# Performance work log

Measured on AMD Instinct MI355X. Metric: run time of the kernel, lower is better.

## Reference

```python
import jax, jax.numpy as jnp
import numpy as np

N, E = 50000, 800000          # nodes, edges
IN_DIM, HID, OUT = 200, 256, 64  # hidden_dims
R = 2                          # num_relations
NEG_SLOPE = 0.2                # RGATConv default negative_slope
EPS = 1e-16                    # PyG softmax denominator eps


def _glorot(key, shape, fan):
    return jax.random.normal(key, shape, dtype=jnp.float32) / np.float32(np.sqrt(fan))


def setup_inputs() -> dict:
    key = jax.random.key(0)
    ks = jax.random.split(key, 13)
    features = jax.random.normal(ks[0], (N, IN_DIM), dtype=jnp.float32)
    edge_index = jax.random.randint(ks[1], (2, E), 0, N, dtype=jnp.int64)
    edge_type = jax.random.randint(ks[2], (E,), 0, R, dtype=jnp.int64)
    return {
        "features": features,
        "edge_index": edge_index,
        "edge_type": edge_type,
        # RGATConv layer 1 (heads=1, dim=1): weight [R, in, out], q/k [out, 1]
        "w1": _glorot(ks[3], (R, IN_DIM, HID), IN_DIM),
        "q1": _glorot(ks[4], (HID, 1), HID),
        "k1": _glorot(ks[5], (HID, 1), HID),
        # RGATConv layer 2
        "w2": _glorot(ks[6], (R, HID, OUT), HID),
        "q2": _glorot(ks[7], (OUT, 1), OUT),
        "k2": _glorot(ks[8], (OUT, 1), OUT),
        # decoder: Linear(OUT->HID) then Linear(HID->IN_DIM), stored as [in, out]
        "dW1": _glorot(ks[9], (OUT, HID), OUT),
        "db1": jnp.zeros((HID,), jnp.float32),
        "dW2": _glorot(ks[10], (HID, IN_DIM), HID),
        "db2": jnp.zeros((IN_DIM,), jnp.float32),
    }


def rgat_conv(x, src, dst, etype, w, q, k):
    """PyG RGATConv: additive-self-attention, across-relation softmax,
    heads=1, dim=1, concat=False, bias=False, aggr=add (eval mode: no dropout)."""
    n = x.shape[0]
    # relation-specific transform at node level (per-edge bmm factors through nodes)
    xw = jnp.einsum('ni,ric->rnc', x, w)          # [R, N, C]
    qn = jnp.einsum('rnc,ch->rnh', xw, q)         # [R, N, 1]
    kn = jnp.einsum('rnc,ch->rnh', xw, k)         # [R, N, 1]
    # per-edge attention logit: leaky_relu(q_i + k_j)
    alpha = jax.nn.leaky_relu(qn[etype, dst] + kn[etype, src], NEG_SLOPE)  # [E, 1]
    # segment softmax over destination nodes (across relations)
    m = jax.lax.stop_gradient(jax.ops.segment_max(alpha, dst, num_segments=n))
    m = jnp.where(jnp.isfinite(m), m, jnp.float32(0.0))
    ea = jnp.exp(alpha - m[dst])
    denom = jax.ops.segment_sum(ea, dst, num_segments=n)
    att = ea / (denom[dst] + EPS)                 # [E, 1]
    # scatter-add weighted messages
    msg = att * xw[etype, src]                    # [E, C]
    return jax.ops.segment_sum(msg, dst, num_segments=n)  # [N, C]


def reference(features, edge_index, edge_type, w1, q1, k1, w2, q2, k2, dW1, db1, dW2, db2):
    src, dst = edge_index[0], edge_index[1]
    h1 = jax.nn.elu(rgat_conv(features, src, dst, edge_type, w1, q1, k1))
    h2 = jax.nn.elu(rgat_conv(h1, src, dst, edge_type, w2, q2, k2))
    h3 = (h2 @ dW1 + db1) @ dW2 + db2   # decoder (PCA mode: no ReLU)
    return (h2, h3)
```

## Files before the change

### kernel.cpp

```cpp
#include <hip/hip_runtime.h>

#define IN_DIM 200
#define HID    256
#define OUT_D  64
#define RREL   2
#define NEG_SLOPE 0.2f
#define NNODE  50000
#define MPAD   50048

typedef __attribute__((ext_vector_type(8))) short bf16x8;
typedef __attribute__((ext_vector_type(4))) float f32x4;
typedef __attribute__((ext_vector_type(4))) unsigned int u32x4;

__device__ __forceinline__ float bf2f(unsigned short u) {
    union { unsigned int i; float f; } v; v.i = ((unsigned int)u) << 16; return v.f;
}
__device__ __forceinline__ unsigned short f2bf(float f) {
    union { float f; unsigned int i; } v; v.f = f;
    unsigned int u = v.i;
    return (unsigned short)((u + 0x7FFFu + ((u >> 16) & 1u)) >> 16);
}
__device__ __forceinline__ float elu(float v) { return v > 0.f ? v : (__expf(v) - 1.0f); }

__global__ void feat_cvt(const float* __restrict__ in, unsigned short* __restrict__ out)
{
    long long idx = (long long)blockIdx.x * 256 + threadIdx.x;
    int row = (int)(idx >> 6);
    int c4  = ((int)idx & 63) << 2;
    if (row >= MPAD) return;
    unsigned short v[4];
    #pragma unroll
    for (int i = 0; i < 4; ++i) {
        int c = c4 + i;
        float f = (row < NNODE && c < IN_DIM) ? in[(long long)row * IN_DIM + c] : 0.f;
        v[i] = f2bf(f);
    }
    *(ushort4*)(out + (long long)row * 256 + c4) = make_ushort4(v[0], v[1], v[2], v[3]);
}

__global__ void wt_cvt(const float* __restrict__ in, unsigned short* __restrict__ out,
                       int Kreal, int Nreal, int Kpad, int Npad, int nb)
{
    long long total = (long long)nb * Npad * Kpad;
    long long idx = (long long)blockIdx.x * 256 + threadIdx.x;
    if (idx >= total) return;
    int kk = (int)(idx % Kpad);
    long long t = idx / Kpad;
    int nrow = (int)(t % Npad);
    int z = (int)(t / Npad);
    float f = (kk < Kreal && nrow < Nreal) ? in[((long long)z * Kreal + kk) * Nreal + nrow] : 0.f;
    out[idx] = f2bf(f);
}

__global__ void wt_cvt_stack(const float* __restrict__ in, unsigned short* __restrict__ out)
{
    int idx = blockIdx.x * 256 + threadIdx.x;
    if (idx >= 2 * 256 * 256) return;
    int kk = idx & 255;
    int c  = (idx >> 8) & 255;
    int z  = idx >> 16;
    float f = (kk < IN_DIM) ? in[((long long)z * IN_DIM + kk) * 256 + c] : 0.f;
    out[(long long)c * 512 + z * 256 + kk] = f2bf(f);
}

__global__ __launch_bounds__(256) void wqk_cvt(
    const float* __restrict__ w, const float* __restrict__ q,
    const float* __restrict__ k, float* __restrict__ wqv, float* __restrict__ wkv)
{
    int wv = ((blockIdx.x << 8) + threadIdx.x) >> 6;
    int lane = threadIdx.x & 63;
    if (wv >= 512) return;
    int r = wv >> 8, kk = wv & 255;
    float sq = 0.f, sk = 0.f;
    if (kk < IN_DIM) {
        const float* row = w + ((long long)(r * IN_DIM + kk)) * 256;
        float4 wv4 = *(const float4*)(row + lane * 4);
        float4 qv4 = *(const float4*)(q + lane * 4);
        float4 kv4 = *(const float4*)(k + lane * 4);
        sq = wv4.x * qv4.x + wv4.y * qv4.y + wv4.z * qv4.z + wv4.w * qv4.w;
        sk = wv4.x * kv4.x + wv4.y * kv4.y + wv4.z * kv4.z + wv4.w * kv4.w;
        #pragma unroll
        for (int off = 32; off; off >>= 1) {
            sq += __shfl_xor(sq, off);
            sk += __shfl_xor(sk, off);
        }
    }
    if (lane == 0) { wqv[r * 256 + kk] = sq; wkv[r * 256 + kk] = sk; }
}

__global__ __launch_bounds__(256) void qk_feat(
    const unsigned short* __restrict__ A1, const float* __restrict__ wqv,
    const float* __restrict__ wkv, float* __restrict__ qn, float* __restrict__ kn, int n)
{
    int wv = ((blockIdx.x << 8) + threadIdx.x) >> 6;
    int lane = threadIdx.x & 63;
    if (wv >= n) return;
    ushort4 v = *(const ushort4*)(A1 + (long long)wv * 256 + lane * 4);
    float x0 = bf2f(v.x), x1 = bf2f(v.y), x2 = bf2f(v.z), x3 = bf2f(v.w);
    float4 q0v = *(const float4*)(wqv + lane * 4);
    float4 k0v = *(const float4*)(wkv + lane * 4);
    float4 q1v = *(const float4*)(wqv + 256 + lane * 4);
    float4 k1v = *(const float4*)(wkv + 256 + lane * 4);
    float sq0 = x0 * q0v.x + x1 * q0v.y + x2 * q0v.z + x3 * q0v.w;
    float sk0 = x0 * k0v.x + x1 * k0v.y + x2 * k0v.z + x3 * k0v.w;
    float sq1 = x0 * q1v.x + x1 * q1v.y + x2 * q1v.z + x3 * q1v.w;
    float sk1 = x0 * k1v.x + x1 * k1v.y + x2 * k1v.z + x3 * k1v.w;
    #pragma unroll
    for (int off = 32; off; off >>= 1) {
        sq0 += __shfl_xor(sq0, off);
        sk0 += __shfl_xor(sk0, off);
        sq1 += __shfl_xor(sq1, off);
        sk1 += __shfl_xor(sk1, off);
    }
    if (lane == 0) {
        qn[wv] = sq0; qn[n + wv] = sq1;
        kn[wv] = sk0; kn[n + wv] = sk1;
    }
}

template<bool OUT_BF16, bool DO_ELU, bool FUSE_QK>
__global__ __launch_bounds__(256) void gemm_mfma(
    const unsigned short* __restrict__ A,
    const unsigned short* __restrict__ Bt,
    const float* __restrict__ bias,
    void* __restrict__ Cout,
    const float* __restrict__ qvec, const float* __restrict__ kvec,
    float* __restrict__ qn_out, float* __restrict__ kn_out,
    int M, int Nn, int Kp, int Npad,
    long long strideC)
{
    __shared__ __align__(16) char lds[49152];
    const int tid  = threadIdx.x;
    const int lane = tid & 63;
    const int w    = tid >> 6;
    const int m0   = blockIdx.x * 128;
    const int n0   = blockIdx.y * 64;
    const int z    = blockIdx.z;

    const char* Ab = (const char*)A;
    const char* Bb = (const char*)(Bt + (long long)z * Npad * Kp);
    const int rs = Kp * 2;

    f32x4 acc[2][4];
    #pragma unroll
    for (int i = 0; i < 2; ++i)
        #pragma unroll
        for (int j = 0; j < 4; ++j) acc[i][j] = (f32x4){0.f, 0.f, 0.f, 0.f};

    const int KT = Kp >> 6;

    auto stage = [&](int buf, int kt) {
        char* lA = lds + buf * 24576;
        char* lB = lA + 16384;
        #pragma unroll
        for (int i = 0; i < 4; ++i) {
            int g = i * 256 + tid;
            int row = g >> 3, c = g & 7;
            const char* src = Ab + (long long)(m0 + row) * rs + kt * 128 + ((c ^ (row & 7)) << 4);
            __builtin_amdgcn_global_load_lds((const __attribute__((address_space(1))) void*)src,
                                             (__attribute__((address_space(3))) void*)(lA + g * 16),
                                             16, 0, 0);
        }
        #pragma unroll
        for (int i = 0; i < 2; ++i) {
            int g = i * 256 + tid;
            int row = g >> 3, c = g & 7;
            const char* src = Bb + (long long)(n0 + row) * rs + kt * 128 + ((c ^ (row & 7)) << 4);
            __builtin_amdgcn_global_load_lds((const __attribute__((address_space(1))) void*)src,
                                             (__attribute__((address_space(3))) void*)(lB + g * 16),
                                             16, 0, 0);
        }
    };

    stage(0, 0);
    int cur = 0;
    for (int kt = 0; kt < KT; ++kt) {
        __syncthreads();
        if (kt + 1 < KT) stage(cur ^ 1, kt + 1);
        const char* lA = lds + cur * 24576;
        const char* lB = lA + 16384;
        #pragma unroll
        for (int ks = 0; ks < 2; ++ks) {
            const int kg = ks * 4 + (lane >> 4);
            bf16x8 a[2], b[4];
            #pragma unroll
            for (int mi = 0; mi < 2; ++mi) {
                int row = w * 32 + mi * 16 + (lane & 15);
                a[mi] = *(const bf16x8*)(lA + row * 128 + ((kg ^ (row & 7)) << 4));
            }
            #pragma unroll
            for (int nj = 0; nj < 4; ++nj) {
                int row = nj * 16 + (lane & 15);
                b[nj] = *(const bf16x8*)(lB + row * 128 + ((kg ^ (row & 7)) << 4));
            }
            #pragma unroll
            for (int mi = 0; mi < 2; ++mi)
                #pragma unroll
                for (int nj = 0; nj < 4; ++nj)
                    acc[mi][nj] = __builtin_amdgcn_mfma_f32_16x16x32_bf16(a[mi], b[nj], acc[mi][nj], 0, 0, 0);
        }
        cur ^= 1;
    }

    const int colb = n0 + (lane & 15);
    #pragma unroll
    for (int mi = 0; mi < 2; ++mi) {
        #pragma unroll
        for (int nj = 0; nj < 4; ++nj) {
            int col = colb + nj * 16;
            if (col >= Nn) continue;
            float badd = bias ? bias[col] : 0.f;
            #pragma unroll
            for (int r = 0; r < 4; ++r) {
                int rowm = m0 + w * 32 + mi * 16 + ((lane >> 4) << 2) + r;
                if (rowm >= M) continue;
                float v = acc[mi][nj][r] + badd;
                if (DO_ELU) v = v > 0.f ? v : (__expf(v) - 1.0f);
                if (OUT_BF16)
                    ((unsigned short*)Cout)[strideC * z + (long long)rowm * Nn + col] = f2bf(v);
                else
                    ((float*)Cout)[strideC * z + (long long)rowm * Nn + col] = v;
            }
        }
    }

    if (FUSE_QK) {
        float qv[4], kv[4];
        #pragma unroll
        for (int nj = 0; nj < 4; ++nj) {
            int col = colb + nj * 16;
            bool ok = col < Nn;
            qv[nj] = ok ? qvec[col] : 0.f;
            kv[nj] = ok ? kvec[col] : 0.f;
        }
        #pragma unroll
        for (int mi = 0; mi < 2; ++mi) {
            #pragma unroll
            for (int r = 0; r < 4; ++r) {
                float sq = 0.f, sk = 0.f;
                #pragma unroll
                for (int nj = 0; nj < 4; ++nj) {
                    sq = fmaf(acc[mi][nj][r], qv[nj], sq);
                    sk = fmaf(acc[mi][nj][r], kv[nj], sk);
                }
                #pragma unroll
                for (int off = 1; off < 16; off <<= 1) {
                    sq += __shfl_xor(sq, off);
                    sk += __shfl_xor(sk, off);
                }
                if ((lane & 15) == 0) {
                    int rowm = m0 + w * 32 + mi * 16 + ((lane >> 4) << 2) + r;
                    if (rowm < M) {
                        atomicAdd(qn_out + (long long)z * M + rowm, sq);
                        atomicAdd(kn_out + (long long)z * M + rowm, sk);
                    }
                }
            }
        }
    }
}

__global__ void count_kernel(const int* __restrict__ dst, const int* __restrict__ etype,
                             int* __restrict__ deg2, int E)
{
    int e = blockIdx.x * 256 + threadIdx.x;
    if (e < E) atomicAdd(&deg2[(dst[e] << 1) | etype[e]], 1);
}

__global__ __launch_bounds__(256) void scan_blocksum(
    const int* __restrict__ deg, int* __restrict__ bsum, int n)
{
    __shared__ int red[256];
    int i = blockIdx.x * 256 + threadIdx.x;
    int v = (i < n) ? deg[i] : 0;
    red[threadIdx.x] = v;
    __syncthreads();
    #pragma unroll
    for (int off = 128; off; off >>= 1) {
        if (threadIdx.x < off) red[threadIdx.x] += red[threadIdx.x + off];
        __syncthreads();
    }
    if (threadIdx.x == 0) bsum[blockIdx.x] = red[0];
}

__global__ __launch_bounds__(512) void scan_bsum(int* __restrict__ bsum, int nb)
{
    __shared__ int buf[512];
    const int t = threadIdx.x;
    int v = (t < nb) ? bsum[t] : 0;
    buf[t] = v;
    __syncthreads();
    #pragma unroll
    for (int off = 1; off < 512; off <<= 1) {
        int u = (t >= off) ? buf[t - off] : 0;
        __syncthreads();
        buf[t] += u;
        __syncthreads();
    }
    if (t < nb) bsum[t] = buf[t] - v;
}

__global__ __launch_bounds__(256) void scan_final(
    const int* __restrict__ deg, const int* __restrict__ bsum,
    int* __restrict__ row_ptr, int* __restrict__ cursor, int n)
{
    __shared__ int buf[256];
    const int t = threadIdx.x;
    const int i = blockIdx.x * 256 + t;
    int v = (i < n) ? deg[i] : 0;
    buf[t] = v;
    __syncthreads();
    #pragma unroll
    for (int off = 1; off < 256; off <<= 1) {
        int u = (t >= off) ? buf[t - off] : 0;
        __syncthreads();
        buf[t] += u;
        __syncthreads();
    }
    int excl = bsum[blockIdx.x] + buf[t] - v;
    if (i < n) { row_ptr[i] = excl; cursor[i] = excl; }
    if (i == n - 1) row_ptr[n] = excl + v;
}

__global__ void scatter_kernel(const int* __restrict__ dst, const int* __restrict__ src,
                               const int* __restrict__ etype, int* __restrict__ cursor2,
                               int* __restrict__ epk, int E)
{
    int e = blockIdx.x * 256 + threadIdx.x;
    if (e < E) {
        int p = atomicAdd(&cursor2[(dst[e] << 1) | etype[e]], 1);
        epk[p] = src[e];
    }
}

__global__ __launch_bounds__(256) void aggregate_z(
    const unsigned short* __restrict__ A1,
    const float* __restrict__ qn,
    const float* __restrict__ kn,
    const int* __restrict__ row_ptr2,
    const int* __restrict__ epk,
    unsigned short* __restrict__ z,
    int n)
{
    const int wv   = ((blockIdx.x << 8) + threadIdx.x) >> 6;
    const int lane = threadIdx.x & 63;
    if (wv >= n) return;
    const int d = wv;
    const int start = row_ptr2[2 * d];
    const int mid   = row_ptr2[2 * d + 1];
    const int end   = row_ptr2[2 * d + 2];
    const int cnt = end - start;
    const int c0  = mid - start;
    const float q0 = qn[d];
    const float q1 = qn[n + d];
    const int slot = lane >> 5;
    const int hl   = lane & 31;

    auto fma8 = [](float acc[8], float w, const u32x4& r) {
        #pragma unroll
        for (int t2 = 0; t2 < 4; ++t2) {
            unsigned dw = r[t2];
            acc[2 * t2]     = fmaf(w, __uint_as_float(dw << 16),         acc[2 * t2]);
            acc[2 * t2 + 1] = fmaf(w, __uint_as_float(dw & 0xFFFF0000u), acc[2 * t2 + 1]);
        }
    };

    if (cnt <= 64) {
        int pv = 0; float a = -INFINITY;
        if (lane < cnt) {
            pv = epk[start + lane];
            bool r1 = lane >= c0;
            a = (r1 ? q1 : q0) + kn[(r1 ? n : 0) + pv];
            a = a > 0.f ? a : NEG_SLOPE * a;
        }
        float mx = a;
        #pragma unroll
        for (int off = 32; off; off >>= 1) mx = fmaxf(mx, __shfl_xor(mx, off));
        float ev = (lane < cnt) ? __expf(a - mx) : 0.f;
        float se = ev;
        #pragma unroll
        for (int off = 32; off; off >>= 1) se += __shfl_xor(se, off);
        const float wvv = ev * (1.f / (se + 1e-16f));

        #pragma unroll
        for (int seg = 0; seg < 2; ++seg) {
            const int segoff = seg ? c0 : 0;
            const int cs = seg ? (cnt - c0) : c0;
            float accA[8], accB[8];
            #pragma unroll
            for (int i = 0; i < 8; ++i) { accA[i] = 0.f; accB[i] = 0.f; }

            const int iters = (cs + 1) >> 1;
            int k = 0;
            for (; k + 4 <= iters; k += 4) {
                const int e0 = slot + k * 2, e1 = e0 + 2, e2 = e0 + 4, e3 = e0 + 6;
                int   p0 = __shfl(pv, segoff + e0);
                float w0 = __shfl(wvv, segoff + e0);
                int   p1 = __shfl(pv, segoff + e1);
                float w1 = __shfl(wvv, segoff + e1);
                int   p2 = __shfl(pv, segoff + e2);
                float w2 = __shfl(wvv, segoff + e2);
                int   p3 = __shfl(pv, segoff + e3);
                float w3 = __shfl(wvv, segoff + e3);
                if (e0 >= cs) w0 = 0.f;
                if (e1 >= cs) w1 = 0.f;
                if (e2 >= cs) w2 = 0.f;
                if (e3 >= cs) w3 = 0.f;
                const u32x4 r0 = *(const u32x4*)(A1 + (long long)p0 * 256 + hl * 8);
                const u32x4 r1 = *(const u32x4*)(A1 + (long long)p1 * 256 + hl * 8);
                const u32x4 r2 = *(const u32x4*)(A1 + (long long)p2 * 256 + hl * 8);
                const u32x4 r3 = *(const u32x4*)(A1 + (long long)p3 * 256 + hl * 8);
                fma8(accA, w0, r0);
                fma8(accB, w1, r1);
                fma8(accA, w2, r2);
                fma8(accB, w3, r3);
            }
            for (; k < iters; ++k) {
                const int e0 = slot + k * 2;
                int   p0 = __shfl(pv, segoff + e0);
                float w0 = __shfl(wvv, segoff + e0);
                if (e0 >= cs) w0 = 0.f;
                const u32x4 r0 = *(const u32x4*)(A1 + (long long)p0 * 256 + hl * 8);
                fma8(accA, w0, r0);
            }

            float acc[8];
            #pragma unroll
            for (int i = 0; i < 8; ++i) acc[i] = accA[i] + accB[i];
            #pragma unroll
            for (int t2 = 0; t2 < 8; ++t2) acc[t2] += __shfl_xor(acc[t2], 32);
            if (slot == 0) {
                u32x4 pack;
                #pragma unroll
                for (int t2 = 0; t2 < 4; ++t2)
                    pack[t2] = (unsigned)f2bf(acc[2 * t2]) | ((unsigned)f2bf(acc[2 * t2 + 1]) << 16);
                *(u32x4*)(z + (long long)d * 512 + seg * 256 + hl * 8) = pack;
            }
        }
        return;
    }

    float mx = -INFINITY;
    for (int j = start + lane; j < end; j += 64) {
        int s = epk[j];
        bool r1 = j >= mid;
        float a = (r1 ? q1 : q0) + kn[(r1 ? n : 0) + s];
        a = a > 0.f ? a : NEG_SLOPE * a;
        mx = fmaxf(mx, a);
    }
    #pragma unroll
    for (int off = 32; off; off >>= 1) mx = fmaxf(mx, __shfl_xor(mx, off));

    float se = 0.f;
    for (int j = start + lane; j < end; j += 64) {
        int s = epk[j];
        bool r1 = j >= mid;
        float a = (r1 ? q1 : q0) + kn[(r1 ? n : 0) + s];
        a = a > 0.f ? a : NEG_SLOPE * a;
        se += __expf(a - mx);
    }
    #pragma unroll
    for (int off = 32; off; off >>= 1) se += __shfl_xor(se, off);
    const float inv = 1.f / (se + 1e-16f);

    #pragma unroll
    for (int seg = 0; seg < 2; ++seg) {
        const int s0 = seg ? mid : start;
        const int s1 = seg ? end : mid;
        const float qr = seg ? q1 : q0;
        const int kbase = seg ? n : 0;

        float accA[8], accB[8];
        #pragma unroll
        for (int i = 0; i < 8; ++i) { accA[i] = 0.f; accB[i] = 0.f; }

        for (int base = s0; base < s1; base += 64) {
            const int cnt2 = min(64, s1 - base);
            int pv = 0; float wvv = 0.f;
            if (lane < cnt2) {
                pv = epk[base + lane];
                float a = qr + kn[kbase + pv];
                a = a > 0.f ? a : NEG_SLOPE * a;
                wvv = __expf(a - mx) * inv;
            }
            const int iters = (cnt2 + 1) >> 1;
            int k = 0;
            for (; k + 2 <= iters; k += 2) {
                const int e0 = slot + k * 2;
                const int e1 = e0 + 2;
                int   pA = __shfl(pv, e0);
                float wA = __shfl(wvv, e0);
                int   pB = __shfl(pv, e1);
                float wB = __shfl(wvv, e1);
                const u32x4 rA = *(const u32x4*)(A1 + (long long)pA * 256 + hl * 8);
                const u32x4 rB = *(const u32x4*)(A1 + (long long)pB * 256 + hl * 8);
                fma8(accA, wA, rA);
                fma8(accB, wB, rB);
            }
            if (k < iters) {
                const int e0 = slot + k * 2;
                int   pA = __shfl(pv, e0);
                float wA = __shfl(wvv, e0);
                const u32x4 rA = *(const u32x4*)(A1 + (long long)pA * 256 + hl * 8);
                fma8(accA, wA, rA);
            }
        }

        float acc[8];
        #pragma unroll
        for (int i = 0; i < 8; ++i) acc[i] = accA[i] + accB[i];
        #pragma unroll
        for (int t2 = 0; t2 < 8; ++t2) acc[t2] += __shfl_xor(acc[t2], 32);

        if (slot == 0) {
            u32x4 pack;
            #pragma unroll
            for (int t2 = 0; t2 < 4; ++t2)
                pack[t2] = (unsigned)f2bf(acc[2 * t2]) | ((unsigned)f2bf(acc[2 * t2 + 1]) << 16);
            *(u32x4*)(z + (long long)d * 512 + seg * 256 + hl * 8) = pack;
        }
    }
}

__global__ __launch_bounds__(256) void aggregate2(
    const unsigned short* __restrict__ xw,
    const float* __restrict__ qn,
    const float* __restrict__ kn,
    const int* __restrict__ row_ptr2,
    const int* __restrict__ epk,
    unsigned short* __restrict__ outb,
    float* __restrict__ outf,
    int n)
{
    constexpr int LPE   = 8;
    constexpr int NSLOT = 8;

    const int wv   = ((blockIdx.x << 8) + threadIdx.x) >> 6;
    const int lane = threadIdx.x & 63;
    if (wv >= n) return;
    const int d = wv;
    const int start = row_ptr2[2 * d];
    const int mid   = row_ptr2[2 * d + 1];
    const int end   = row_ptr2[2 * d + 2];
    const int cnt = end - start;
    const int c0  = mid - start;
    const float q0 = qn[d];
    const float q1 = qn[n + d];
    const int slot = lane / LPE;
    const int hl   = lane % LPE;

    auto fma8 = [](float acc[8], float w, const u32x4& r) {
        #pragma unroll
        for (int t2 = 0; t2 < 4; ++t2) {
            unsigned dw = r[t2];
            acc[2 * t2]     = fmaf(w, __uint_as_float(dw << 16),         acc[2 * t2]);
            acc[2 * t2 + 1] = fmaf(w, __uint_as_float(dw & 0xFFFF0000u), acc[2 * t2 + 1]);
        }
    };

    float accA[8], accB[8];
    #pragma unroll
    for (int i = 0; i < 8; ++i) { accA[i] = 0.f; accB[i] = 0.f; }

    if (cnt <= 64) {
        int pv = 0; float a = -INFINITY;
        if (lane < cnt) {
            pv = epk[start + lane];
            bool r1 = lane >= c0;
            a = (r1 ? q1 : q0) + kn[(r1 ? n : 0) + pv];
            a = a > 0.f ? a : NEG_SLOPE * a;
        }
        float mx = a;
        #pragma unroll
        for (int off = 32; off; off >>= 1) mx = fmaxf(mx, __shfl_xor(mx, off));
        float ev = (lane < cnt) ? __expf(a - mx) : 0.f;
        float se = ev;
        #pragma unroll
        for (int off = 32; off; off >>= 1) se += __shfl_xor(se, off);
        const float wvn = ev * (1.f / (se + 1e-16f));

        const int iters = (cnt + NSLOT - 1) / NSLOT;
        int k = 0;
        for (; k + 2 <= iters; k += 2) {
            const int e0 = slot + k * NSLOT;
            const int e1 = e0 + NSLOT;
            int   pA = __shfl(pv, e0);
            float wA = __shfl(wvn, e0);
            int   pB = __shfl(pv, e1);
            float wB = __shfl(wvn, e1);
            const long long oA = ((e0 >= c0) ? (long long)MPAD * 64 : 0) + (long long)pA * 64 + hl * 8;
            const long long oB = ((e1 >= c0) ? (long long)MPAD * 64 : 0) + (long long)pB * 64 + hl * 8;
            const u32x4 rA = *(const u32x4*)(xw + oA);
            const u32x4 rB = *(const u32x4*)(xw + oB);
            fma8(accA, wA, rA);
            fma8(accB, wB, rB);
        }
        if (k < iters) {
            const int e0 = slot + k * NSLOT;
            int   pA = __shfl(pv, e0);
            float wA = __shfl(wvn, e0);
            const long long oA = ((e0 >= c0) ? (long long)MPAD * 64 : 0) + (long long)pA * 64 + hl * 8;
            const u32x4 rA = *(const u32x4*)(xw + oA);
            fma8(accA, wA, rA);
        }
    } else {
        float mx = -INFINITY;
        for (int j = start + lane; j < end; j += 64) {
            int s = epk[j];
            bool r1 = j >= mid;
            float a = (r1 ? q1 : q0) + kn[(r1 ? n : 0) + s];
            a = a > 0.f ? a : NEG_SLOPE * a;
            mx = fmaxf(mx, a);
        }
        #pragma unroll
        for (int off = 32; off; off >>= 1) mx = fmaxf(mx, __shfl_xor(mx, off));

        float se = 0.f;
        for (int j = start + lane; j < end; j += 64) {
            int s = epk[j];
            bool r1 = j >= mid;
            float a = (r1 ? q1 : q0) + kn[(r1 ? n : 0) + s];
            a = a > 0.f ? a : NEG_SLOPE * a;
            se += __expf(a - mx);
        }
        #pragma unroll
        for (int off = 32; off; off >>= 1) se += __shfl_xor(se, off);
        const float inv = 1.f / (se + 1e-16f);

        for (int base = start; base < end; base += 64) {
            const int cnt2 = min(64, end - base);
            int pv = 0; float wvn = 0.f;
            if (lane < cnt2) {
                int j = base + lane;
                pv = epk[j];
                bool r1 = j >= mid;
                float a = (r1 ? q1 : q0) + kn[(r1 ? n : 0) + pv];
                a = a > 0.f ? a : NEG_SLOPE * a;
                wvn = __expf(a - mx) * inv;
            }
            const int iters = (cnt2 + NSLOT - 1) / NSLOT;
            int k = 0;
            for (; k + 2 <= iters; k += 2) {
                const int e0 = slot + k * NSLOT;
                const int e1 = e0 + NSLOT;
                int   pA = __shfl(pv, e0);
                float wA = __shfl(wvn, e0);
                int   pB = __shfl(pv, e1);
                float wB = __shfl(wvn, e1);
                const long long oA = ((base + e0 >= mid) ? (long long)MPAD * 64 : 0) + (long long)pA * 64 + hl * 8;
                const long long oB = ((base + e1 >= mid) ? (long long)MPAD * 64 : 0) + (long long)pB * 64 + hl * 8;
                const u32x4 rA = *(const u32x4*)(xw + oA);
                const u32x4 rB = *(const u32x4*)(xw + oB);
                fma8(accA, wA, rA);
                fma8(accB, wB, rB);
            }
            if (k < iters) {
                const int e0 = slot + k * NSLOT;
                int   pA = __shfl(pv, e0);
                float wA = __shfl(wvn, e0);
                const long long oA = ((base + e0 >= mid) ? (long long)MPAD * 64 : 0) + (long long)pA * 64 + hl * 8;
                const u32x4 rA = *(const u32x4*)(xw + oA);
                fma8(accA, wA, rA);
            }
        }
    }

    float acc[8];
    #pragma unroll
    for (int i = 0; i < 8; ++i) acc[i] = accA[i] + accB[i];
    #pragma unroll
    for (int off = LPE; off < 64; off <<= 1)
        #pragma unroll
        for (int t2 = 0; t2 < 8; ++t2) acc[t2] += __shfl_xor(acc[t2], off);

    if (slot == 0) {
        float fo[8];
        #pragma unroll
        for (int t2 = 0; t2 < 8; ++t2) fo[t2] = elu(acc[t2]);
        u32x4 pack;
        #pragma unroll
        for (int t2 = 0; t2 < 4; ++t2)
            pack[t2] = (unsigned)f2bf(fo[2 * t2]) | ((unsigned)f2bf(fo[2 * t2 + 1]) << 16);
        *(u32x4*)(outb + (long long)d * 64 + hl * 8) = pack;
        *(float4*)(outf + (long long)d * 64 + hl * 8)     = make_float4(fo[0], fo[1], fo[2], fo[3]);
        *(float4*)(outf + (long long)d * 64 + hl * 8 + 4) = make_float4(fo[4], fo[5], fo[6], fo[7]);
    }
}

extern "C" void kernel_launch(void* const* d_in, const int* in_sizes, int n_in,
                              void* d_out, int out_size, void* d_ws, size_t ws_size,
                              hipStream_t stream)
{
    const float* features = (const float*)d_in[0];
    const int*   ei       = (const int*)d_in[1];
    const int*   etype    = (const int*)d_in[2];
    const float* w1       = (const float*)d_in[3];
    const float* q1       = (const float*)d_in[4];
    const float* k1       = (const float*)d_in[5];
    const float* w2       = (const float*)d_in[6];
    const float* q2       = (const float*)d_in[7];
    const float* k2       = (const float*)d_in[8];
    const float* dW1      = (const float*)d_in[9];
    const float* db1      = (const float*)d_in[10];
    const float* dW2      = (const float*)d_in[11];
    const float* db2      = (const float*)d_in[12];

    const int n = in_sizes[0] / IN_DIM;
    const int E = in_sizes[2];
    const int n2 = 2 * n;
    const int* src = ei;
    const int* dst = ei + E;

    float* out_h2 = (float*)d_out;
    float* out_h3 = out_h2 + (long long)n * OUT_D;

    char* wp = (char*)d_ws;
    auto carve = [&](size_t bytes) {
        char* p = wp; wp += (bytes + 255) & ~(size_t)255; return p;
    };
    unsigned short* A1   = (unsigned short*)carve((size_t)MPAD * 256 * 2);
    unsigned short* zbuf = (unsigned short*)carve((size_t)MPAD * 512 * 2);
    unsigned short* h1   = (unsigned short*)carve((size_t)MPAD * 256 * 2);
    unsigned short* xw2  = (unsigned short*)carve((size_t)2 * MPAD * 64 * 2);
    unsigned short* h2b  = (unsigned short*)carve((size_t)MPAD * 64 * 2);
    unsigned short* tdec = (unsigned short*)carve((size_t)MPAD * 256 * 2);
    unsigned short* wst  = (unsigned short*)carve((size_t)256 * 512 * 2);
    unsigned short* w2t  = (unsigned short*)carve((size_t)2 * 64 * 256 * 2);
    unsigned short* dW1t = (unsigned short*)carve((size_t)256 * 64 * 2);
    unsigned short* dW2t = (unsigned short*)carve((size_t)256 * 256 * 2);
    float* wqv    = (float*)carve((size_t)2 * 256 * 4);
    float* wkv    = (float*)carve((size_t)2 * 256 * 4);
    float* qnb    = (float*)carve((size_t)n2 * 4);
    float* knb    = (float*)carve((size_t)n2 * 4);
    int* row_ptr2 = (int*)carve((size_t)(n2 + 1) * 4);
    int* cursor2  = (int*)carve((size_t)n2 * 4);
    int* deg2     = (int*)carve((size_t)n2 * 4);
    int* bsum     = (int*)carve((size_t)512 * 4);
    int* epk      = (int*)carve((size_t)E * 4);

    const int EB  = (E + 255) / 256;
    const int NB2 = (n2 + 255) / 256;
    const int MB  = (n + 127) / 128;
    const int WAVE_N  = (n + 3) / 4;

    hipMemsetAsync(deg2, 0, (size_t)n2 * sizeof(int), stream);
    count_kernel<<<EB, 256, 0, stream>>>(dst, etype, deg2, E);
    scan_blocksum<<<NB2, 256, 0, stream>>>(deg2, bsum, n2);
    scan_bsum<<<1, 512, 0, stream>>>(bsum, NB2);
    scan_final<<<NB2, 256, 0, stream>>>(deg2, bsum, row_ptr2, cursor2, n2);
    scatter_kernel<<<EB, 256, 0, stream>>>(dst, src, etype, cursor2, epk, E);

    feat_cvt<<<(MPAD * 64 + 255) / 256, 256, 0, stream>>>(features, A1);
    wt_cvt_stack<<<(2 * 256 * 256 + 255) / 256, 256, 0, stream>>>(w1, wst);
    wt_cvt<<<(2 * 64 * 256 + 255) / 256, 256, 0, stream>>>(w2, w2t, HID, OUT_D, 256, 64, RREL);
    wt_cvt<<<(256 * 64 + 255) / 256, 256, 0, stream>>>(dW1, dW1t, OUT_D, HID, 64, 256, 1);
    wt_cvt<<<(256 * 256 + 255) / 256, 256, 0, stream>>>(dW2, dW2t, HID, IN_DIM, 256, 256, 1);
    wqk_cvt<<<128, 256, 0, stream>>>(w1, q1, k1, wqv, wkv);

    qk_feat<<<WAVE_N, 256, 0, stream>>>(A1, wqv, wkv, qnb, knb, n);
    aggregate_z<<<WAVE_N, 256, 0, stream>>>(A1, qnb, knb, row_ptr2, epk, zbuf, n);
    {
        dim3 g(MB, 4, 1);
        gemm_mfma<true, true, false><<<g, 256, 0, stream>>>(zbuf, wst, nullptr, h1,
                                                            nullptr, nullptr, nullptr, nullptr,
                                                            n, HID, 512, 256, 0);
    }

    hipMemsetAsync(qnb, 0, (size_t)n2 * 4, stream);
    hipMemsetAsync(knb, 0, (size_t)n2 * 4, stream);
    {
        dim3 g(MB, 1, RREL);
        gemm_mfma<true, false, true><<<g, 256, 0, stream>>>(h1, w2t, nullptr, xw2,
                                                            q2, k2, qnb, knb,
                                                            n, OUT_D, 256, 64, (long long)MPAD * OUT_D);
    }
    aggregate2<<<WAVE_N, 256, 0, stream>>>(xw2, qnb, knb, row_ptr2, epk,
                                           h2b, out_h2, n);

    {
        dim3 g(MB, 4, 1);
        gemm_mfma<true, false, false><<<g, 256, 0, stream>>>(h2b, dW1t, db1, tdec,
                                                             nullptr, nullptr, nullptr, nullptr,
                                                             n, HID, 64, 256, 0);
    }
    {
        dim3 g(MB, 4, 1);
        gemm_mfma<false, false, false><<<g, 256, 0, stream>>>(tdec, dW2t, db2, out_h3,
                                                              nullptr, nullptr, nullptr, nullptr,
                                                              n, IN_DIM, 256, 256, 0);
    }
}
```

Measured before the change: 351.4 us.

## Merge prep kernels and memsets into one launch; interleave relation segments in aggregation

Folds the feature/weight conversion kernels, the wq/wk precompute and the three memsets into a single block-partitioned prep kernel. Separate q/k buffers for layer 2 let their zeroing move into that prep kernel. The small-degree path of aggregate_z now walks both relation segments in one loop with packed float2 accumulators, so the two segments' gathers overlap instead of running in two sequential passes. This cuts launch count and adds memory-level parallelism, at the cost of wasted loads when the two segments are unbalanced.

```diff
diff --git a/kernel.cpp b/kernel.cpp
--- a/kernel.cpp
+++ b/kernel.cpp
@@ -10,6 +10,7 @@
 
 typedef __attribute__((ext_vector_type(8))) short bf16x8;
 typedef __attribute__((ext_vector_type(4))) float f32x4;
+typedef __attribute__((ext_vector_type(2))) float f32x2;
 typedef __attribute__((ext_vector_type(4))) unsigned int u32x4;
 
 __device__ __forceinline__ float bf2f(unsigned short u) {
@@ -22,27 +23,11 @@
 }
 __device__ __forceinline__ float elu(float v) { return v > 0.f ? v : (__expf(v) - 1.0f); }
 
-__global__ void feat_cvt(const float* __restrict__ in, unsigned short* __restrict__ out)
-{
-    long long idx = (long long)blockIdx.x * 256 + threadIdx.x;
-    int row = (int)(idx >> 6);
-    int c4  = ((int)idx & 63) << 2;
-    if (row >= MPAD) return;
-    unsigned short v[4];
-    #pragma unroll
-    for (int i = 0; i < 4; ++i) {
-        int c = c4 + i;
-        float f = (row < NNODE && c < IN_DIM) ? in[(long long)row * IN_DIM + c] : 0.f;
-        v[i] = f2bf(f);
-    }
-    *(ushort4*)(out + (long long)row * 256 + c4) = make_ushort4(v[0], v[1], v[2], v[3]);
-}
-
-__global__ void wt_cvt(const float* __restrict__ in, unsigned short* __restrict__ out,
-                       int Kreal, int Nreal, int Kpad, int Npad, int nb)
+__device__ __forceinline__ void wt_cvt_body(
+    const float* __restrict__ in, unsigned short* __restrict__ out,
+    int Kreal, int Nreal, int Kpad, int Npad, int nb, long long idx)
 {
     long long total = (long long)nb * Npad * Kpad;
-    long long idx = (long long)blockIdx.x * 256 + threadIdx.x;
     if (idx >= total) return;
     int kk = (int)(idx % Kpad);
     long long t = idx / Kpad;
@@ -52,40 +37,83 @@
     out[idx] = f2bf(f);
 }
 
-__global__ void wt_cvt_stack(const float* __restrict__ in, unsigned short* __restrict__ out)
-{
-    int idx = blockIdx.x * 256 + threadIdx.x;
-    if (idx >= 2 * 256 * 256) return;
-    int kk = idx & 255;
-    int c  = (idx >> 8) & 255;
-    int z  = idx >> 16;
-    float f = (kk < IN_DIM) ? in[((long long)z * IN_DIM + kk) * 256 + c] : 0.f;
-    out[(long long)c * 512 + z * 256 + kk] = f2bf(f);
-}
-
-__global__ __launch_bounds__(256) void wqk_cvt(
-    const float* __restrict__ w, const float* __restrict__ q,
-    const float* __restrict__ k, float* __restrict__ wqv, float* __restrict__ wkv)
-{
-    int wv = ((blockIdx.x << 8) + threadIdx.x) >> 6;
-    int lane = threadIdx.x & 63;
-    if (wv >= 512) return;
-    int r = wv >> 8, kk = wv & 255;
-    float sq = 0.f, sk = 0.f;
-    if (kk < IN_DIM) {
-        const float* row = w + ((long long)(r * IN_DIM + kk)) * 256;
-        float4 wv4 = *(const float4*)(row + lane * 4);
-        float4 qv4 = *(const float4*)(q + lane * 4);
-        float4 kv4 = *(const float4*)(k + lane * 4);
-        sq = wv4.x * qv4.x + wv4.y * qv4.y + wv4.z * qv4.z + wv4.w * qv4.w;
-        sk = wv4.x * kv4.x + wv4.y * kv4.y + wv4.z * kv4.z + wv4.w * kv4.w;
-        #pragma unroll
-        for (int off = 32; off; off >>= 1) {
-            sq += __shfl_xor(sq, off);
-            sk += __shfl_xor(sk, off);
-        }
-    }
-    if (lane == 0) { wqv[r * 256 + kk] = sq; wkv[r * 256 + kk] = sk; }
+#define PB_FEAT   12512
+#define PB_WST    (PB_FEAT + 512)
+#define PB_W2T    (PB_WST + 128)
+#define PB_DW1    (PB_W2T + 64)
+#define PB_DW2    (PB_DW1 + 256)
+#define PB_WQK    (PB_DW2 + 128)
+#define PB_DEG    (PB_WQK + 391)
+#define PB_QK2    (PB_DEG + 391)
+
+__global__ __launch_bounds__(256) void prep_all(
+    const float* __restrict__ features, const float* __restrict__ w1,
+    const float* __restrict__ w2, const float* __restrict__ dW1,
+    const float* __restrict__ dW2, const float* __restrict__ q1,
+    const float* __restrict__ k1,
+    unsigned short* __restrict__ A1, unsigned short* __restrict__ wst,
+    unsigned short* __restrict__ w2t, unsigned short* __restrict__ dW1t,
+    unsigned short* __restrict__ dW2t, float* __restrict__ wqv,
+    float* __restrict__ wkv, int* __restrict__ deg2,
+    float* __restrict__ qnb2, float* __restrict__ knb2, int n2)
+{
+    const int b = blockIdx.x;
+    const int tid = threadIdx.x;
+
+    if (b < PB_FEAT) {
+        long long idx = (long long)b * 256 + tid;
+        int row = (int)(idx >> 6);
+        int c4  = ((int)idx & 63) << 2;
+        if (row >= MPAD) return;
+        unsigned short v[4];
+        #pragma unroll
+        for (int i = 0; i < 4; ++i) {
+            int c = c4 + i;
+            float f = (row < NNODE && c < IN_DIM) ? features[(long long)row * IN_DIM + c] : 0.f;
+            v[i] = f2bf(f);
+        }
+        *(ushort4*)(A1 + (long long)row * 256 + c4) = make_ushort4(v[0], v[1], v[2], v[3]);
+    } else if (b < PB_WST) {
+        int idx = (b - PB_FEAT) * 256 + tid;
+        if (idx >= 2 * 256 * 256) return;
+        int kk = idx & 255;
+        int c  = (idx >> 8) & 255;
+        int z  = idx >> 16;
+        float f = (kk < IN_DIM) ? w1[((long long)z * IN_DIM + kk) * 256 + c] : 0.f;
+        wst[(long long)c * 512 + z * 256 + kk] = f2bf(f);
+    } else if (b < PB_W2T) {
+        wt_cvt_body(w2, w2t, HID, OUT_D, 256, 64, RREL, (long long)(b - PB_WST) * 256 + tid);
+    } else if (b < PB_DW1) {
+        wt_cvt_body(dW1, dW1t, OUT_D, HID, 64, 256, 1, (long long)(b - PB_W2T) * 256 + tid);
+    } else if (b < PB_DW2) {
+        wt_cvt_body(dW2, dW2t, HID, IN_DIM, 256, 256, 1, (long long)(b - PB_DW1) * 256 + tid);
+    } else if (b < PB_WQK) {
+        int wv = (((b - PB_DW2) << 8) + tid) >> 6;
+        int lane = tid & 63;
+        if (wv >= 512) return;
+        int r = wv >> 8, kk = wv & 255;
+        float sq = 0.f, sk = 0.f;
+        if (kk < IN_DIM) {
+            const float* row = w1 + ((long long)(r * IN_DIM + kk)) * 256;
+            float4 wv4 = *(const float4*)(row + lane * 4);
+            float4 qv4 = *(const float4*)(q1 + lane * 4);
+            float4 kv4 = *(const float4*)(k1 + lane * 4);
+            sq = wv4.x * qv4.x + wv4.y * qv4.y + wv4.z * qv4.z + wv4.w * qv4.w;
+            sk = wv4.x * kv4.x + wv4.y * kv4.y + wv4.z * kv4.z + wv4.w * kv4.w;
+            #pragma unroll
+            for (int off = 32; off; off >>= 1) {
+                sq += __shfl_xor(sq, off);
+                sk += __shfl_xor(sk, off);
+            }
+        }
+        if (lane == 0) { wqv[r * 256 + kk] = sq; wkv[r * 256 + kk] = sk; }
+    } else if (b < PB_DEG) {
+        int i = (b - PB_WQK) * 256 + tid;
+        if (i < n2) deg2[i] = 0;
+    } else if (b < PB_QK2) {
+        int i = (b - PB_DEG) * 256 + tid;
+        if (i < n2) { qnb2[i] = 0.f; knb2[i] = 0.f; }
+    }
 }
 
 __global__ __launch_bounds__(256) void qk_feat(
@@ -356,7 +384,16 @@
     const int slot = lane >> 5;
     const int hl   = lane & 31;
 
-    auto fma8 = [](float acc[8], float w, const u32x4& r) {
+    auto fma8v = [](f32x2 acc[4], float w, const u32x4& r) {
+        #pragma unroll
+        for (int t2 = 0; t2 < 4; ++t2) {
+            f32x2 x;
+            x.x = __uint_as_float(r[t2] << 16);
+            x.y = __uint_as_float(r[t2] & 0xFFFF0000u);
+            acc[t2] += w * x;
+        }
+    };
+    auto fma8s = [](float acc[8], float w, const u32x4& r) {
         #pragma unroll
         for (int t2 = 0; t2 < 4; ++t2) {
             unsigned dw = r[t2];
@@ -382,60 +419,64 @@
         for (int off = 32; off; off >>= 1) se += __shfl_xor(se, off);
         const float wvv = ev * (1.f / (se + 1e-16f));
 
-        #pragma unroll
-        for (int seg = 0; seg < 2; ++seg) {
-            const int segoff = seg ? c0 : 0;
-            const int cs = seg ? (cnt - c0) : c0;
-            float accA[8], accB[8];
+        const int cs0 = c0, cs1 = cnt - c0;
+        const int it0 = (cs0 + 1) >> 1, it1 = (cs1 + 1) >> 1;
+        const int itmax = max(it0, it1);
+
+        f32x2 acc0[4], acc1[4];
+        #pragma unroll
+        for (int i = 0; i < 4; ++i) { acc0[i] = (f32x2){0.f, 0.f}; acc1[i] = (f32x2){0.f, 0.f}; }
+
+        int k = 0;
+        for (; k + 2 <= itmax; k += 2) {
+            const int e00 = slot + k * 2, e01 = e00 + 2;
+            int   p00 = __shfl(pv, e00);               float w00 = __shfl(wvv, e00);
+            int   p01 = __shfl(pv, e01);               float w01 = __shfl(wvv, e01);
+            const int s10 = min(c0 + e00, 63), s11 = min(c0 + e01, 63);
+            int   p10 = __shfl(pv, s10);               float w10 = __shfl(wvv, s10);
+            int   p11 = __shfl(pv, s11);               float w11 = __shfl(wvv, s11);
+            if (e00 >= cs0) { w00 = 0.f; p00 = 0; }
+            if (e01 >= cs0) { w01 = 0.f; p01 = 0; }
+            if (e00 >= cs1) { w10 = 0.f; p10 = 0; }
+            if (e01 >= cs1) { w11 = 0.f; p11 = 0; }
+            const u32x4 r00 = *(const u32x4*)(A1 + (long long)p00 * 256 + hl * 8);
+            const u32x4 r10 = *(const u32x4*)(A1 + (long long)p10 * 256 + hl * 8);
+            const u32x4 r01 = *(const u32x4*)(A1 + (long long)p01 * 256 + hl * 8);
+            const u32x4 r11 = *(const u32x4*)(A1 + (long long)p11 * 256 + hl * 8);
+            fma8v(acc0, w00, r00);
+            fma8v(acc1, w10, r10);
+            fma8v(acc0, w01, r01);
+            fma8v(acc1, w11, r11);
+        }
+        if (k < itmax) {
+            const int e00 = slot + k * 2;
+            int   p00 = __shfl(pv, e00);               float w00 = __shfl(wvv, e00);
+            const int s10 = min(c0 + e00, 63);
+            int   p10 = __shfl(pv, s10);               float w10 = __shfl(wvv, s10);
+            if (e00 >= cs0) { w00 = 0.f; p00 = 0; }
+            if (e00 >= cs1) { w10 = 0.f; p10 = 0; }
+            const u32x4 r00 = *(const u32x4*)(A1 + (long long)p00 * 256 + hl * 8);
+            const u32x4 r10 = *(const u32x4*)(A1 + (long long)p10 * 256 + hl * 8);
+            fma8v(acc0, w00, r00);
+            fma8v(acc1, w10, r10);
+        }
+
+        #pragma unroll
+        for (int t2 = 0; t2 < 4; ++t2) {
+            acc0[t2].x += __shfl_xor(acc0[t2].x, 32);
+            acc0[t2].y += __shfl_xor(acc0[t2].y, 32);
+            acc1[t2].x += __shfl_xor(acc1[t2].x, 32);
+            acc1[t2].y += __shfl_xor(acc1[t2].y, 32);
+        }
+        if (slot == 0) {
+            u32x4 pack0, pack1;
             #pragma unroll
-            for (int i = 0; i < 8; ++i) { accA[i] = 0.f; accB[i] = 0.f; }
-
-            const int iters = (cs + 1) >> 1;
-            int k = 0;
-            for (; k + 4 <= iters; k += 4) {
-                const int e0 = slot + k * 2, e1 = e0 + 2, e2 = e0 + 4, e3 = e0 + 6;
-                int   p0 = __shfl(pv, segoff + e0);
-                float w0 = __shfl(wvv, segoff + e0);
-                int   p1 = __shfl(pv, segoff + e1);
-                float w1 = __shfl(wvv, segoff + e1);
-                int   p2 = __shfl(pv, segoff + e2);
-                float w2 = __shfl(wvv, segoff + e2);
-                int   p3 = __shfl(pv, segoff + e3);
-                float w3 = __shfl(wvv, segoff + e3);
-                if (e0 >= cs) w0 = 0.f;
-                if (e1 >= cs) w1 = 0.f;
-                if (e2 >= cs) w2 = 0.f;
-                if (e3 >= cs) w3 = 0.f;
-                const u32x4 r0 = *(const u32x4*)(A1 + (long long)p0 * 256 + hl * 8);
-                const u32x4 r1 = *(const u32x4*)(A1 + (long long)p1 * 256 + hl * 8);
-                const u32x4 r2 = *(const u32x4*)(A1 + (long long)p2 * 256 + hl * 8);
-                const u32x4 r3 = *(const u32x4*)(A1 + (long long)p3 * 256 + hl * 8);
-                fma8(accA, w0, r0);
-                fma8(accB, w1, r1);
-                fma8(accA, w2, r2);
-                fma8(accB, w3, r3);
-            }
-            for (; k < iters; ++k) {
-                const int e0 = slot + k * 2;
-                int   p0 = __shfl(pv, segoff + e0);
-                float w0 = __shfl(wvv, segoff + e0);
-                if (e0 >= cs) w0 = 0.f;
-                const u32x4 r0 = *(const u32x4*)(A1 + (long long)p0 * 256 + hl * 8);
-                fma8(accA, w0, r0);
-            }
-
-            float acc[8];
-            #pragma unroll
-            for (int i = 0; i < 8; ++i) acc[i] = accA[i] + accB[i];
-            #pragma unroll
-            for (int t2 = 0; t2 < 8; ++t2) acc[t2] += __shfl_xor(acc[t2], 32);
-            if (slot == 0) {
-                u32x4 pack;
-                #pragma unroll
-                for (int t2 = 0; t2 < 4; ++t2)
-                    pack[t2] = (unsigned)f2bf(acc[2 * t2]) | ((unsigned)f2bf(acc[2 * t2 + 1]) << 16);
-                *(u32x4*)(z + (long long)d * 512 + seg * 256 + hl * 8) = pack;
-            }
+            for (int t2 = 0; t2 < 4; ++t2) {
+                pack0[t2] = (unsigned)f2bf(acc0[t2].x) | ((unsigned)f2bf(acc0[t2].y) << 16);
+                pack1[t2] = (unsigned)f2bf(acc1[t2].x) | ((unsigned)f2bf(acc1[t2].y) << 16);
+            }
+            *(u32x4*)(z + (long long)d * 512 + hl * 8)       = pack0;
+            *(u32x4*)(z + (long long)d * 512 + 256 + hl * 8) = pack1;
         }
         return;
     }
@@ -494,15 +535,15 @@
                 float wB = __shfl(wvv, e1);
                 const u32x4 rA = *(const u32x4*)(A1 + (long long)pA * 256 + hl * 8);
                 const u32x4 rB = *(const u32x4*)(A1 + (long long)pB * 256 + hl * 8);
-                fma8(accA, wA, rA);
-                fma8(accB, wB, rB);
+                fma8s(accA, wA, rA);
+                fma8s(accB, wB, rB);
             }
             if (k < iters) {
                 const int e0 = slot + k * 2;
                 int   pA = __shfl(pv, e0);
                 float wA = __shfl(wvv, e0);
                 const u32x4 rA = *(const u32x4*)(A1 + (long long)pA * 256 + hl * 8);
-                fma8(accA, wA, rA);
+                fma8s(accA, wA, rA);
             }
         }
 
@@ -730,8 +771,10 @@
     unsigned short* dW2t = (unsigned short*)carve((size_t)256 * 256 * 2);
     float* wqv    = (float*)carve((size_t)2 * 256 * 4);
     float* wkv    = (float*)carve((size_t)2 * 256 * 4);
-    float* qnb    = (float*)carve((size_t)n2 * 4);
-    float* knb    = (float*)carve((size_t)n2 * 4);
+    float* qnb1   = (float*)carve((size_t)n2 * 4);
+    float* knb1   = (float*)carve((size_t)n2 * 4);
+    float* qnb2   = (float*)carve((size_t)n2 * 4);
+    float* knb2   = (float*)carve((size_t)n2 * 4);
     int* row_ptr2 = (int*)carve((size_t)(n2 + 1) * 4);
     int* cursor2  = (int*)carve((size_t)n2 * 4);
     int* deg2     = (int*)carve((size_t)n2 * 4);
@@ -741,24 +784,20 @@
     const int EB  = (E + 255) / 256;
     const int NB2 = (n2 + 255) / 256;
     const int MB  = (n + 127) / 128;
-    const int WAVE_N  = (n + 3) / 4;
-
-    hipMemsetAsync(deg2, 0, (size_t)n2 * sizeof(int), stream);
+    const int WAVE_N = (n + 3) / 4;
+
+    prep_all<<<PB_QK2, 256, 0, stream>>>(features, w1, w2, dW1, dW2, q1, k1,
+                                         A1, wst, w2t, dW1t, dW2t,
+                                         wqv, wkv, deg2, qnb2, knb2, n2);
+
     count_kernel<<<EB, 256, 0, stream>>>(dst, etype, deg2, E);
     scan_blocksum<<<NB2, 256, 0, stream>>>(deg2, bsum, n2);
     scan_bsum<<<1, 512, 0, stream>>>(bsum, NB2);
     scan_final<<<NB2, 256, 0, stream>>>(deg2, bsum, row_ptr2, cursor2, n2);
     scatter_kernel<<<EB, 256, 0, stream>>>(dst, src, etype, cursor2, epk, E);
 
-    feat_cvt<<<(MPAD * 64 + 255) / 256, 256, 0, stream>>>(features, A1);
-    wt_cvt_stack<<<(2 * 256 * 256 + 255) / 256, 256, 0, stream>>>(w1, wst);
-    wt_cvt<<<(2 * 64 * 256 + 255) / 256, 256, 0, stream>>>(w2, w2t, HID, OUT_D, 256, 64, RREL);
-    wt_cvt<<<(256 * 64 + 255) / 256, 256, 0, stream>>>(dW1, dW1t, OUT_D, HID, 64, 256, 1);
-    wt_cvt<<<(256 * 256 + 255) / 256, 256, 0, stream>>>(dW2, dW2t, HID, IN_DIM, 256, 256, 1);
-    wqk_cvt<<<128, 256, 0, stream>>>(w1, q1, k1, wqv, wkv);
-
-    qk_feat<<<WAVE_N, 256, 0, stream>>>(A1, wqv, wkv, qnb, knb, n);
-    aggregate_z<<<WAVE_N, 256, 0, stream>>>(A1, qnb, knb, row_ptr2, epk, zbuf, n);
+    qk_feat<<<WAVE_N, 256, 0, stream>>>(A1, wqv, wkv, qnb1, knb1, n);
+    aggregate_z<<<WAVE_N, 256, 0, stream>>>(A1, qnb1, knb1, row_ptr2, epk, zbuf, n);
     {
         dim3 g(MB, 4, 1);
         gemm_mfma<true, true, false><<<g, 256, 0, stream>>>(zbuf, wst, nullptr, h1,
@@ -766,15 +805,13 @@
                                                             n, HID, 512, 256, 0);
     }
 
-    hipMemsetAsync(qnb, 0, (size_t)n2 * 4, stream);
-    hipMemsetAsync(knb, 0, (size_t)n2 * 4, stream);
     {
         dim3 g(MB, 1, RREL);
         gemm_mfma<true, false, true><<<g, 256, 0, stream>>>(h1, w2t, nullptr, xw2,
-                                                            q2, k2, qnb, knb,
+                                                            q2, k2, qnb2, knb2,
                                                             n, OUT_D, 256, 64, (long long)MPAD * OUT_D);
     }
-    aggregate2<<<WAVE_N, 256, 0, stream>>>(xw2, qnb, knb, row_ptr2, epk,
+    aggregate2<<<WAVE_N, 256, 0, stream>>>(xw2, qnb2, knb2, row_ptr2, epk,
                                            h2b, out_h2, n);
 
     {
```

Measured after the change: 333.9 us. 1.05x faster.
